# Performance work log

Hardware: AMD Instinct MI355X
Metric: run time of the kernel (lower is better)

Reference implementation:

```python
import jax, jax.numpy as jnp
import numpy as np

K = 3
STRIDE = 1
PAD = 1


def setup_inputs() -> dict:
    key = jax.random.key(0)
    k1, k2, k3 = jax.random.split(key, 3)
    N, C, H, W = 4, 256, 64, 64
    outC = 256
    x = jax.random.normal(k1, (N, C, H, W), dtype=jnp.float32)
    # offset/mask conv params (torch inits these to 0; small random makes the test nontrivial)
    conv_offset_w = jax.random.normal(k2, (3 * K * K, C, K, K), dtype=jnp.float32) * 0.01
    conv_offset_b = jnp.zeros((3 * K * K,), dtype=jnp.float32)
    # xavier-normal scale for dcn weight
    fan = C * K * K + outC * K * K
    dcn_weight = jax.random.normal(k3, (outC, C, K, K), dtype=jnp.float32) * np.float32(np.sqrt(2.0 / fan))
    return {"x": x, "conv_offset_w": conv_offset_w, "conv_offset_b": conv_offset_b, "dcn_weight": dcn_weight}


def _dcn(x, w_off, b_off, dcn_weight):
    k, s, p = K, STRIDE, PAD
    N, C, H, W = x.shape
    outC = dcn_weight.shape[0]
    KK = k * k
    # offset/mask prediction conv
    om = jax.lax.conv_general_dilated(
        x, w_off, (s, s), [(p, p), (p, p)],
        dimension_numbers=("NCHW", "OIHW", "NCHW")) + b_off[None, :, None, None]
    offset = om[:, : 2 * KK]
    mask = jax.nn.sigmoid(om[:, 2 * KK:])
    oH = (H + 2 * p - (k - 1)) // s
    oW = (W + 2 * p - (k - 1)) // s
    # pad with an extra row/col at bottom-right so floor+1 indexing is in-bounds (as in torch code)
    px = jnp.pad(x, ((0, 0), (0, 0), (p, p + 1), (p, p + 1)))
    px = jnp.transpose(px, (0, 2, 3, 1))  # (N, H+2p+1, W+2p+1, C)
    offset = jnp.transpose(offset, (0, 2, 3, 1)).reshape(N, oH, oW, KK, 2)  # (...,(y,x))
    mask = jnp.transpose(mask, (0, 2, 3, 1))  # (N, oH, oW, KK)
    base_y = jnp.arange(oH, dtype=jnp.float32) * s + p
    base_x = jnp.arange(oW, dtype=jnp.float32) * s + p
    half = (k - 1) // 2
    inner_y = jnp.repeat(jnp.arange(k, dtype=jnp.float32) - half, k)  # kernel-tap y offsets
    inner_x = jnp.tile(jnp.arange(k, dtype=jnp.float32) - half, k)   # kernel-tap x offsets
    pos_y = base_y[None, :, None, None] + inner_y[None, None, None, :] + offset[..., 0]
    pos_x = base_x[None, None, :, None] + inner_x[None, None, None, :] + offset[..., 1]
    pos_y = jnp.clip(pos_y, 0.0, H + 2 * p - 1.0)
    pos_x = jnp.clip(pos_x, 0.0, W + 2 * p - 1.0)
    y1 = jnp.floor(pos_y)
    x1 = jnp.floor(pos_x)
    y1i = y1.astype(jnp.int32)
    x1i = x1.astype(jnp.int32)
    nidx = jnp.arange(N)[:, None, None, None]
    # bilinear gathers: each (N, oH, oW, KK, C)
    v1 = px[nidx, y1i, x1i]
    v2 = px[nidx, y1i, x1i + 1]
    v3 = px[nidx, y1i + 1, x1i]
    v4 = px[nidx, y1i + 1, x1i + 1]
    lh = (pos_y - y1)[..., None]
    lw = (pos_x - x1)[..., None]
    hh = 1.0 - lh
    hw = 1.0 - lw
    value = hh * hw * v1 + hh * lw * v2 + lh * hw * v3 + lh * lw * v4
    value = value * mask[..., None]  # modulated
    w = dcn_weight.reshape(outC, C, KK)
    # sum over in_C and kernel taps -> NCHW output
    out = jnp.einsum("nhwkc,ock->nohw", value, w)
    return out


def reference(x, conv_offset_w, conv_offset_b, dcn_weight):
    return _dcn(x, conv_offset_w, conv_offset_b, dcn_weight)
```

## Files before the change

### kernel.cpp

```cpp
#include <hip/hip_runtime.h>
#include <type_traits>


typedef __bf16 bf16x8 __attribute__((ext_vector_type(8)));
typedef float  f32x4  __attribute__((ext_vector_type(4)));
typedef unsigned short ushort8 __attribute__((ext_vector_type(8)));
typedef unsigned int   uint4v  __attribute__((ext_vector_type(4)));

#define XBF_OFF   0u
#define WREP_OFF  8388608u
#define WMAIN_OFF 8536064u

#define LGKM0_BAR() do { __builtin_amdgcn_s_waitcnt(0xC07F); __builtin_amdgcn_s_barrier(); } while (0)

template <int N> using ic = std::integral_constant<int, N>;

__device__ __forceinline__ unsigned short f2bf(float f) {
  unsigned int u = __float_as_uint(f);
  u += 0x7fffu + ((u >> 16) & 1u);
  return (unsigned short)(u >> 16);
}
__device__ __forceinline__ float bf2f(unsigned short h) {
  return __uint_as_float(((unsigned int)h) << 16);
}

__global__ __launch_bounds__(256) void k_pre(const float* __restrict__ x,
                                             const float* __restrict__ w_off,
                                             const float* __restrict__ dcn_w,
                                             unsigned short* __restrict__ xbf,
                                             unsigned short* __restrict__ wrep,
                                             unsigned short* __restrict__ wmain) {
  __shared__ float tile[32][65];
  __shared__ unsigned short lsh[2304];
  int b = blockIdx.x;
  int t = threadIdx.x;
  if (b < 2048) {
    int n  = b >> 9;
    int cb = (b >> 6) & 7;
    int xb = b & 63;
    int xx  = t & 63;
    int cc0 = t >> 6;
#pragma unroll
    for (int j = 0; j < 8; ++j) {
      int cc = cc0 + j * 4;
      tile[cc][xx] = x[((size_t)(n * 256 + cb * 32 + cc) << 12) + xb * 64 + xx];
    }
    __syncthreads();
    int ccw = t & 31;
    int xw0 = t >> 5;
#pragma unroll
    for (int j = 0; j < 8; ++j) {
      int xw = xw0 + j * 8;
      xbf[((size_t)((n << 12) + xb * 64 + xw)) * 256 + cb * 32 + ccw] = f2bf(tile[ccw][xw]);
    }
  } else {
    int ocb = b - 2048;
    if (ocb < 32) {
      int oc = ocb;
      if (oc >= 27) {
#pragma unroll
        for (int j = 0; j < 9; ++j) wrep[oc * 2304 + j * 256 + t] = 0;
        return;
      }
      const float* base = w_off + (size_t)oc * 2304;
#pragma unroll
      for (int j = 0; j < 9; ++j) lsh[j * 256 + t] = f2bf(base[t * 9 + j]);
      __syncthreads();
#pragma unroll
      for (int j = 0; j < 9; ++j) wrep[oc * 2304 + j * 256 + t] = lsh[j * 256 + t];
    } else {
      int oc = ocb - 32;
      const float* base = dcn_w + (size_t)oc * 2304;
      int oco = ((oc >> 4) << 9) + (oc & 15) * 8;
#pragma unroll
      for (int j = 0; j < 9; ++j) {
        int k = j * 256 + t;
        wmain[((k >> 5) << 13) + oco + (((k >> 3) & 3) << 7) + (k & 7)] =
            f2bf(base[t * 9 + j]);
      }
    }
  }
}

__global__ __launch_bounds__(1024, 4) void k_gemm_fused(const unsigned short* __restrict__ xbf,
                                                        const unsigned short* __restrict__ wrep,
                                                        const float* __restrict__ bias,
                                                        const unsigned short* __restrict__ wB,
                                                        float* __restrict__ out) {
  __shared__ __align__(16) unsigned char smem[98304];
  __shared__ __align__(16) float om_lds[64 * 32];
  int t = threadIdx.x;
  int wave = t >> 6, lane = t & 63;
  int bm = ((blockIdx.x & 7) << 5) + (blockIdx.x >> 3);
  int n = bm >> 6, oy = bm & 63;
  int mr = lane & 15, q = lane >> 4;

  {
    auto SHa = reinterpret_cast<unsigned short (*)[2][64 * 64]>(smem);
    auto SHb = reinterpret_cast<unsigned short (*)[2][32 * 64]>(smem + 65536);
    int grp = wave >> 2, wv = wave & 3;
    int tg = t & 255;

    unsigned short (*As)[64 * 64] = SHa[grp];
    unsigned short (*Bs)[32 * 64] = SHb[grp];

    int arow = tg >> 2, acc4 = tg & 3;
    int brow = tg >> 3, bch = tg & 7;

    f32x4 acc0 = {0.f, 0.f, 0.f, 0.f};
    f32x4 acc1 = {0.f, 0.f, 0.f, 0.f};

    ushort8 av[2][2]; ushort8 bv[2];
    auto prefetch = [&](int ktg, auto slotc) {
      constexpr int slot = decltype(slotc)::value;
      int kk = ktg >> 2;
      int c0 = (ktg & 3) * 64;
      int dy = kk / 3 - 1, dx = kk % 3 - 1;
      int yy = oy + dy, xxg = arow + dx;
      bool ok = ((unsigned)yy < 64u) && ((unsigned)xxg < 64u);
      const unsigned short* p = xbf + (size_t)(((n * 64 + yy) * 64 + xxg) * 256 + c0 + acc4 * 16);
#pragma unroll
      for (int g = 0; g < 2; ++g)
        av[slot][g] = ok ? *(const ushort8*)(p + g * 8) : (ushort8){0,0,0,0,0,0,0,0};
      bv[slot] = *(const ushort8*)(wrep + (size_t)brow * 2304 + ktg * 64 + bch * 8);
    };

    int k0 = grp * 9;
    prefetch(k0, ic<0>{});
    prefetch(k0 + 1, ic<1>{});

    auto step = [&](int kt, auto slotc) {
      constexpr int slot = decltype(slotc)::value;
#pragma unroll
      for (int g = 0; g < 2; ++g) {
        int ch = (acc4 * 2 + g) ^ (arow & 7);
        *(ushort8*)&As[slot][arow * 64 + ch * 8] = av[slot][g];
      }
      { int ch = bch ^ (brow & 7);
        *(ushort8*)&Bs[slot][brow * 64 + ch * 8] = bv[slot]; }
      if (kt + 2 < 9) prefetch(k0 + kt + 2, slotc);
      LGKM0_BAR();
#pragma unroll
      for (int kh = 0; kh < 2; ++kh) {
        int coff = ((q + kh * 4) ^ (mr & 7)) * 8;
        bf16x8 a  = *(const bf16x8*)&As[slot][(wv * 16 + mr) * 64 + coff];
        bf16x8 b0 = *(const bf16x8*)&Bs[slot][mr * 64 + coff];
        bf16x8 b1 = *(const bf16x8*)&Bs[slot][(16 + mr) * 64 + coff];
        acc0 = __builtin_amdgcn_mfma_f32_16x16x32_bf16(a, b0, acc0, 0, 0, 0);
        acc1 = __builtin_amdgcn_mfma_f32_16x16x32_bf16(a, b1, acc1, 0, 0, 0);
      }
    };
    for (int kp = 0; kp < 4; ++kp) {
      step(2 * kp, ic<0>{});
      step(2 * kp + 1, ic<1>{});
    }
    step(8, ic<0>{});

    float* scratch = (float*)smem;
    __syncthreads();
    if (grp > 0) {
#pragma unroll
      for (int nt = 0; nt < 2; ++nt) {
        f32x4 a = nt ? acc1 : acc0;
#pragma unroll
        for (int rg = 0; rg < 4; ++rg)
          scratch[(grp - 1) * 2048 + (wv * 16 + q * 4 + rg) * 32 + nt * 16 + mr] = a[rg];
      }
    }
    __syncthreads();
    if (grp == 0) {
#pragma unroll
      for (int nt = 0; nt < 2; ++nt) {
        f32x4 a = nt ? acc1 : acc0;
        int oc = nt * 16 + mr;
        float bvl = (oc < 27) ? bias[oc] : 0.f;
#pragma unroll
        for (int rg = 0; rg < 4; ++rg) {
          int pl = wv * 16 + q * 4 + rg;
          float v = a[rg] + bvl + scratch[pl * 32 + oc] +
                    scratch[2048 + pl * 32 + oc] + scratch[4096 + pl * 32 + oc];
          if (oc >= 18 && oc < 27) v = 1.f / (1.f + __expf(-v));
          om_lds[pl * 32 + oc] = v;
        }
      }
    }
  }
  __syncthreads();

  auto Ab = reinterpret_cast<unsigned short (*)[64 * 128]>(smem);
  int r0 = bm * 64;

  if (wave < 8) {
    const unsigned short* Bg = wB + wave * 1024 + lane * 8;
    f32x4 acc[4][2];
#pragma unroll
    for (int mt = 0; mt < 4; ++mt)
#pragma unroll
      for (int nt = 0; nt < 2; ++nt) acc[mt][nt] = (f32x4){0.f, 0.f, 0.f, 0.f};

    bf16x8 bfr[2][4];

    auto issueB = [&](int ks, auto slotc) {
      constexpr int slot = decltype(slotc)::value;
#pragma unroll
      for (int kh = 0; kh < 2; ++kh)
#pragma unroll
        for (int nt = 0; nt < 2; ++nt)
          bfr[slot][kh * 2 + nt] =
              *(const bf16x8*)(Bg + (size_t)(ks * 2 + kh) * 8192 + nt * 512);
    };
    auto mfma64 = [&](auto halfc, auto bufc) {
      constexpr int half = decltype(halfc)::value;
      constexpr int buf  = decltype(bufc)::value;
      __builtin_amdgcn_s_setprio(1);
#pragma unroll
      for (int kh = 0; kh < 2; ++kh) {
        int coff = half * 64 + ((q + kh * 4) ^ (mr & 7)) * 8;
        bf16x8 af[4];
#pragma unroll
        for (int mt = 0; mt < 4; ++mt)
          af[mt] = *(const bf16x8*)&Ab[buf][(mt * 16 + mr) * 128 + coff];
#pragma unroll
        for (int mt = 0; mt < 4; ++mt)
#pragma unroll
          for (int nt = 0; nt < 2; ++nt)
            acc[mt][nt] = __builtin_amdgcn_mfma_f32_16x16x32_bf16(
                af[mt], bfr[half][kh * 2 + nt], acc[mt][nt], 0, 0, 0);
      }
      __builtin_amdgcn_s_setprio(0);
    };

    issueB(0, ic<0>{});
    LGKM0_BAR();
    auto cphase = [&](int p, auto bufc) {
      issueB(2 * p - 1, ic<1>{});
      mfma64(ic<0>{}, bufc);
      if (2 * p < 36) issueB(2 * p, ic<0>{});
      mfma64(ic<1>{}, bufc);
      LGKM0_BAR();
    };
    for (int pp = 0; pp < 9; ++pp) {
      cphase(2 * pp + 1, ic<0>{});
      cphase(2 * pp + 2, ic<1>{});
    }

#pragma unroll
    for (int mt = 0; mt < 4; ++mt)
#pragma unroll
      for (int nt = 0; nt < 2; ++nt) {
        int p = r0 + mt * 16 + q * 4;
        int o = wave * 32 + nt * 16 + mr;
        int nn = p >> 12, pyx = p & 4095;
        *(f32x4*)(out + ((size_t)(nn * 256 + o) << 12) + pyx) = acc[mt][nt];
      }
  } else {
    int pt = t - 512;
    int srow = pt >> 3, sch = (pt & 7) * 8;
    int r = r0 + srow;
    int rn = r >> 12, yx = r & 4095, poy = yx >> 6, pox = yx & 63;
    const unsigned short* xb = xbf + (size_t)rn * (4096 * 256);
    const float* omr = om_lds + srow * 32;
    int wchA = (((pt & 7) ^ (srow & 7)) << 3);

    float pv_y, pv_x, pv_m;
    float cw1, cw2, cw3, cw4;
    int a1, a2, a3, a4;
    float wbuf[2][4];
    ushort8 g1[2], g2[2], g3[2], g4[2];

    auto loadom = [&](int kk) {
      pv_y = omr[2 * kk]; pv_x = omr[2 * kk + 1]; pv_m = omr[18 + kk];
    };
    auto params = [&](int kk) {
      float py = (float)(poy + kk / 3) + pv_y;
      float px = (float)(pox + kk % 3) + pv_x;
      float m = pv_m;
      py = fminf(fmaxf(py, 0.f), 65.f);
      px = fminf(fmaxf(px, 0.f), 65.f);
      float fy = floorf(py), fx = floorf(px);
      float ly = py - fy, lx = px - fx;
      float hy = 1.f - ly, hx = 1.f - lx;
      int iy = (int)fy, ix = (int)fx;
      bool yv0 = (iy >= 1) && (iy <= 64);
      bool yv1 = (iy <= 63);
      bool xv0 = (ix >= 1) && (ix <= 64);
      bool xv1 = (ix <= 63);
      int y0 = min(max(iy - 1, 0), 63);
      int y1 = min(iy, 63);
      int x0 = min(max(ix - 1, 0), 63);
      int x1 = min(ix, 63);
      cw1 = (yv0 && xv0) ? hy * hx * m : 0.f;
      cw2 = (yv0 && xv1) ? hy * lx * m : 0.f;
      cw3 = (yv1 && xv0) ? ly * hx * m : 0.f;
      cw4 = (yv1 && xv1) ? ly * lx * m : 0.f;
      a1 = ((y0 << 6) + x0) * 256;
      a2 = ((y0 << 6) + x1) * 256;
      a3 = ((y1 << 6) + x0) * 256;
      a4 = ((y1 << 6) + x1) * 256;
    };

    auto issueA = [&](int ktg, auto slotc) {
      constexpr int slot = decltype(slotc)::value;
      wbuf[slot][0] = cw1; wbuf[slot][1] = cw2; wbuf[slot][2] = cw3; wbuf[slot][3] = cw4;
      int c = (ktg & 3) * 64 + sch;
      g1[slot] = *(const ushort8*)(xb + a1 + c);
      g2[slot] = *(const ushort8*)(xb + a2 + c);
      g3[slot] = *(const ushort8*)(xb + a3 + c);
      g4[slot] = *(const ushort8*)(xb + a4 + c);
    };
    auto blend = [&](auto slotc, auto halfc, auto bufc) {
      constexpr int slot = decltype(slotc)::value;
      constexpr int half = decltype(halfc)::value;
      constexpr int buf  = decltype(bufc)::value;
      uint4v rs;
#pragma unroll
      for (int pp = 0; pp < 4; ++pp) {
        float va = wbuf[slot][0] * bf2f(g1[slot][2 * pp])     + wbuf[slot][1] * bf2f(g2[slot][2 * pp]) +
                   wbuf[slot][2] * bf2f(g3[slot][2 * pp])     + wbuf[slot][3] * bf2f(g4[slot][2 * pp]);
        float vb = wbuf[slot][0] * bf2f(g1[slot][2 * pp + 1]) + wbuf[slot][1] * bf2f(g2[slot][2 * pp + 1]) +
                   wbuf[slot][2] * bf2f(g3[slot][2 * pp + 1]) + wbuf[slot][3] * bf2f(g4[slot][2 * pp + 1]);
        unsigned ua = __float_as_uint(va) + 0x8000u;
        unsigned ub = __float_as_uint(vb) + 0x8000u;
        rs[pp] = __builtin_amdgcn_perm(ub, ua, 0x07060302u);
      }
      *(uint4v*)&Ab[buf][srow * 128 + half * 64 + wchA] = rs;
    };

    loadom(0);
    params(0);
    loadom(1);
    issueA(0, ic<0>{});
    issueA(1, ic<1>{});

    auto pphase = [&](int p, auto bufc) {
      blend(ic<0>{}, ic<0>{}, bufc);
      {
        int ksn = 2 * p + 2;
        if (ksn < 36) {
          if ((ksn & 3) == 0) {
            int kk = ksn >> 2;
            params(kk);
            loadom(kk < 8 ? kk + 1 : 8);
          }
          issueA(ksn, ic<0>{});
        }
      }
      blend(ic<1>{}, ic<1>{}, bufc);
      {
        int ksn = 2 * p + 3;
        if (ksn < 36) issueA(ksn, ic<1>{});
      }
      LGKM0_BAR();
    };
    for (int pp = 0; pp < 9; ++pp) {
      pphase(2 * pp,     ic<0>{});
      pphase(2 * pp + 1, ic<1>{});
    }
    LGKM0_BAR();
  }
}

extern "C" void kernel_launch(void* const* d_in, const int* in_sizes, int n_in,
                              void* d_out, int out_size, void* d_ws, size_t ws_size,
                              hipStream_t stream) {
  const float* x     = (const float*)d_in[0];
  const float* w_off = (const float*)d_in[1];
  const float* b_off = (const float*)d_in[2];
  const float* dcn_w = (const float*)d_in[3];
  float* out = (float*)d_out;
  char* ws = (char*)d_ws;
  unsigned short* xbf   = (unsigned short*)(ws + XBF_OFF);
  unsigned short* wrep  = (unsigned short*)(ws + WREP_OFF);
  unsigned short* wmain = (unsigned short*)(ws + WMAIN_OFF);

  k_pre<<<2048 + 288, 256, 0, stream>>>(x, w_off, dcn_w, xbf, wrep, wmain);
  k_gemm_fused<<<256, 1024, 0, stream>>>(xbf, wrep, b_off, wmain, out);
}
```

Baseline: 111.3 us.

## Double the per-phase K chunk to halve barriers in the producer/consumer pipeline

Each pipeline phase now stages a full 256-channel kernel tap (four 64-wide quarters) in LDS instead of two, so the producer and MFMA waves meet at a barrier 9 times instead of 18. Producer waves keep four gather slots in flight and compute sampling params once per tap. The aim is to cut barrier and sync overhead and give the gathers deeper latency hiding. In exchange it doubles the LDS A-buffer size and raises register pressure in the gather waves, which could lower occupancy.

Measured after the change: 111.9 us. About the same (+0.6%).

```diff
diff --git a/kernel.cpp b/kernel.cpp
--- a/kernel.cpp
+++ b/kernel.cpp
@@ -187,7 +187,7 @@
   }
   __syncthreads();
 
-  auto Ab = reinterpret_cast<unsigned short (*)[64 * 128]>(smem);
+  auto Ab = reinterpret_cast<unsigned short (*)[64 * 256]>(smem);
   int r0 = bm * 64;
 
   if (wave < 8) {
@@ -209,23 +209,24 @@
           bfr[slot][kh * 2 + nt] =
               *(const bf16x8*)(Bg + (size_t)(ks * 2 + kh) * 8192 + nt * 512);
     };
-    auto mfma64 = [&](auto halfc, auto bufc) {
-      constexpr int half = decltype(halfc)::value;
-      constexpr int buf  = decltype(bufc)::value;
+    auto mfma64 = [&](auto quarterc, auto bufc) {
+      constexpr int quarter = decltype(quarterc)::value;
+      constexpr int slot    = quarter & 1;
+      constexpr int buf     = decltype(bufc)::value;
       __builtin_amdgcn_s_setprio(1);
 #pragma unroll
       for (int kh = 0; kh < 2; ++kh) {
-        int coff = half * 64 + ((q + kh * 4) ^ (mr & 7)) * 8;
+        int coff = quarter * 64 + ((q + kh * 4) ^ (mr & 7)) * 8;
         bf16x8 af[4];
 #pragma unroll
         for (int mt = 0; mt < 4; ++mt)
-          af[mt] = *(const bf16x8*)&Ab[buf][(mt * 16 + mr) * 128 + coff];
+          af[mt] = *(const bf16x8*)&Ab[buf][(mt * 16 + mr) * 256 + coff];
 #pragma unroll
         for (int mt = 0; mt < 4; ++mt)
 #pragma unroll
           for (int nt = 0; nt < 2; ++nt)
             acc[mt][nt] = __builtin_amdgcn_mfma_f32_16x16x32_bf16(
-                af[mt], bfr[half][kh * 2 + nt], acc[mt][nt], 0, 0, 0);
+                af[mt], bfr[slot][kh * 2 + nt], acc[mt][nt], 0, 0, 0);
       }
       __builtin_amdgcn_s_setprio(0);
     };
@@ -233,16 +234,22 @@
     issueB(0, ic<0>{});
     LGKM0_BAR();
     auto cphase = [&](int p, auto bufc) {
-      issueB(2 * p - 1, ic<1>{});
+      int m = 4 * (p - 1);
+      issueB(m + 1, ic<1>{});
       mfma64(ic<0>{}, bufc);
-      if (2 * p < 36) issueB(2 * p, ic<0>{});
+      issueB(m + 2, ic<0>{});
       mfma64(ic<1>{}, bufc);
+      issueB(m + 3, ic<1>{});
+      mfma64(ic<2>{}, bufc);
+      if (m + 4 < 36) issueB(m + 4, ic<0>{});
+      mfma64(ic<3>{}, bufc);
       LGKM0_BAR();
     };
-    for (int pp = 0; pp < 9; ++pp) {
+    for (int pp = 0; pp < 4; ++pp) {
       cphase(2 * pp + 1, ic<0>{});
       cphase(2 * pp + 2, ic<1>{});
     }
+    cphase(9, ic<0>{});
 
 #pragma unroll
     for (int mt = 0; mt < 4; ++mt)
@@ -265,8 +272,8 @@
     float pv_y, pv_x, pv_m;
     float cw1, cw2, cw3, cw4;
     int a1, a2, a3, a4;
-    float wbuf[2][4];
-    ushort8 g1[2], g2[2], g3[2], g4[2];
+    float wbuf[4][4];
+    ushort8 g1[4], g2[4], g3[4], g4[4];
 
     auto loadom = [&](int kk) {
       pv_y = omr[2 * kk]; pv_x = omr[2 * kk + 1]; pv_m = omr[18 + kk];
@@ -308,10 +315,10 @@
       g3[slot] = *(const ushort8*)(xb + a3 + c);
       g4[slot] = *(const ushort8*)(xb + a4 + c);
     };
-    auto blend = [&](auto slotc, auto halfc, auto bufc) {
-      constexpr int slot = decltype(slotc)::value;
-      constexpr int half = decltype(halfc)::value;
-      constexpr int buf  = decltype(bufc)::value;
+    auto blend = [&](auto slotc, auto quarterc, auto bufc) {
+      constexpr int slot    = decltype(slotc)::value;
+      constexpr int quarter = decltype(quarterc)::value;
+      constexpr int buf     = decltype(bufc)::value;
       uint4v rs;
 #pragma unroll
       for (int pp = 0; pp < 4; ++pp) {
@@ -323,7 +330,7 @@
         unsigned ub = __float_as_uint(vb) + 0x8000u;
         rs[pp] = __builtin_amdgcn_perm(ub, ua, 0x07060302u);
       }
-      *(uint4v*)&Ab[buf][srow * 128 + half * 64 + wchA] = rs;
+      *(uint4v*)&Ab[buf][srow * 256 + quarter * 64 + wchA] = rs;
     };
 
     loadom(0);
@@ -331,31 +338,29 @@
     loadom(1);
     issueA(0, ic<0>{});
     issueA(1, ic<1>{});
+    issueA(2, ic<2>{});
+    issueA(3, ic<3>{});
 
     auto pphase = [&](int p, auto bufc) {
       blend(ic<0>{}, ic<0>{}, bufc);
-      {
-        int ksn = 2 * p + 2;
-        if (ksn < 36) {
-          if ((ksn & 3) == 0) {
-            int kk = ksn >> 2;
-            params(kk);
-            loadom(kk < 8 ? kk + 1 : 8);
-          }
-          issueA(ksn, ic<0>{});
-        }
+      if (p < 8) {
+        params(p + 1);
+        loadom(p + 2 <= 8 ? p + 2 : 8);
+        issueA(4 * p + 4, ic<0>{});
       }
       blend(ic<1>{}, ic<1>{}, bufc);
-      {
-        int ksn = 2 * p + 3;
-        if (ksn < 36) issueA(ksn, ic<1>{});
-      }
+      if (p < 8) issueA(4 * p + 5, ic<1>{});
+      blend(ic<2>{}, ic<2>{}, bufc);
+      if (p < 8) issueA(4 * p + 6, ic<2>{});
+      blend(ic<3>{}, ic<3>{}, bufc);
+      if (p < 8) issueA(4 * p + 7, ic<3>{});
       LGKM0_BAR();
     };
-    for (int pp = 0; pp < 9; ++pp) {
+    for (int pp = 0; pp < 4; ++pp) {
       pphase(2 * pp,     ic<0>{});
       pphase(2 * pp + 1, ic<1>{});
     }
+    pphase(8, ic<0>{});
     LGKM0_BAR();
   }
 }
```
